# Kernel tuning notes

Hardware: AMD Instinct MI355X
Metric: run time of the kernel (lower is better)

Reference implementation:

```python
import jax, jax.numpy as jnp
import numpy as np

DIM = 64
NUM_USER = 100000
NUM_ITEM = 100000


def softmax_stable(x, mask=None, axis=-1):
    # exp(x - max) + 1e-10, optional multiplicative mask, normalize
    x = x - jax.lax.stop_gradient(jnp.max(x, axis=axis, keepdims=True))
    e = jnp.exp(x) + 1e-10
    if mask is not None:
        e = e * mask
    return e / jnp.sum(e, axis=axis, keepdims=True)


def setup_inputs() -> dict:
    key = jax.random.key(0)
    ks = jax.random.split(key, 16)
    B, S, L, N, dim = 32, 20, 50, 40000, DIM

    def emb_table(k, n):
        t = jax.random.normal(k, (n + 1, dim), jnp.float32) * 0.02
        return t.at[0].set(0.0)  # padding_idx=0

    def lin(k, fan_in, fan_out):
        s = 1.0 / np.sqrt(fan_in)
        kw, kb = jax.random.split(k)
        W = jax.random.uniform(kw, (fan_in, fan_out), jnp.float32, -s, s)
        b = jax.random.uniform(kb, (fan_out,), jnp.float32, -s, s)
        return W, b

    ue_w1, ue_b1 = lin(ks[7], 2 * dim, dim)      # attn_uencoder layer 1
    ue_w2, ue_b2 = lin(ks[8], dim, 1)            # attn_uencoder layer 2
    uenc_w, uenc_b = lin(ks[9], 2 * dim, dim)    # user_encoder_mlp
    pw, pb = lin(ks[10], 3 * dim, 1)             # predictor_mlp2

    return {
        "user_ids": jax.random.randint(ks[0], (B,), 1, NUM_USER + 1),
        "sess_item": jax.random.randint(ks[1], (B, S), 1, NUM_ITEM + 1),
        "rcnt_item": jax.random.randint(ks[2], (B, L), 1, NUM_ITEM + 1),
        "items_to_predict": jax.random.randint(ks[3], (B, N), 1, NUM_ITEM + 1),
        "item_emb": emb_table(ks[4], NUM_ITEM),
        "user_emb": emb_table(ks[5], NUM_USER),
        "user_emb2": emb_table(ks[6], NUM_USER),
        "ue_w1": ue_w1, "ue_b1": ue_b1,
        "ue_w2": ue_w2, "ue_b2": ue_b2,
        "uenc_w": uenc_w, "uenc_b": uenc_b,
        "pred_w": pw[:, 0], "pred_b": pb[0],
    }


def _forward(user_ids, sess_item, rcnt_item, items_to_predict,
             item_emb, user_emb, user_emb2,
             ue_w1, ue_b1, ue_w2, ue_b2, uenc_w, uenc_b, pred_w, pred_b):
    dim = item_emb.shape[-1]

    # ---- user_encoder7: attention over recent items, fused with user emb ----
    uemb = user_emb[user_ids]                      # [B, d]
    hs = item_emb[rcnt_item]                       # [B, L, d]
    rmask = (rcnt_item != 0)[..., None].astype(hs.dtype)
    cat = jnp.concatenate([jnp.broadcast_to(uemb[:, None, :], hs.shape), hs], axis=-1)
    w = jax.nn.relu(cat @ ue_w1 + ue_b1) @ ue_w2 + ue_b2   # [B, L, 1]
    w = softmax_stable(w, rmask, axis=1)
    hr = jnp.sum(w * hs, axis=1)                   # [B, d]
    hu = jnp.concatenate([user_emb2[user_ids], hr], axis=-1) @ uenc_w + uenc_b  # [B, d]

    # ---- session_encoder (attn_last): self-attention over session items ----
    e = item_emb[sess_item]                        # [B, S, d]
    smask = (sess_item != 0)
    attn_mask = (smask[:, :, None] & smask[:, None, :]).astype(e.dtype)
    logits = jnp.einsum('bsd,btd->bst', e, e) / jnp.sqrt(jnp.asarray(dim, e.dtype))
    a = softmax_stable(logits, attn_mask, axis=-1)
    hc = jnp.einsum('bst,btd->bsd', a, e)          # [B, S, d]

    # ---- predictor_attn, fused: Linear(3d,1) over the virtual [B,S,N,3d]
    # concat == three small projections + broadcast add (identical math) ----
    vemb = item_emb[items_to_predict]              # [B, N, d]
    wu, wc, wv = pred_w[:dim], pred_w[dim:2 * dim], pred_w[2 * dim:]
    g = (hu @ wu)[:, None, None] + (hc @ wc)[:, :, None] \
        + (vemb @ wv)[:, None, :] + pred_b          # [B, S, N]
    attn = jax.nn.sigmoid(g)

    # scores = ((attn*hu + (1-attn)*hc) * vemb).sum(-1), without building h
    hu_v = jnp.einsum('bd,bnd->bn', hu, vemb)       # [B, N]
    hc_v = jnp.einsum('bsd,bnd->bsn', hc, vemb)     # [B, S, N]
    scores = attn * hu_v[:, None, :] + (1.0 - attn) * hc_v
    return scores, hu, hc, attn[..., None]


def reference(user_ids, sess_item, rcnt_item, items_to_predict,
              item_emb, user_emb, user_emb2,
              ue_w1, ue_b1, ue_w2, ue_b2, uenc_w, uenc_b, pred_w, pred_b):
    return _forward(user_ids, sess_item, rcnt_item, items_to_predict,
                    item_emb, user_emb, user_emb2,
                    ue_w1, ue_b1, ue_w2, ue_b2, uenc_w, uenc_b, pred_w, pred_b)
```

## Files before the change

kernel.cpp:

```cpp
#include <hip/hip_runtime.h>
#include <hip/hip_bf16.h>
#include <math.h>

#define BB 32
#define SS 20
#define LL 50
#define NN 40000
#define DD 64
#define TBL_ROWS 100001

#define OFF_SCORES 0
#define OFF_HU     (BB * SS * NN)
#define OFF_HC     (OFF_HU + BB * DD)
#define OFF_ATTN   (OFF_HC + BB * SS * DD)

#define WS_COMB_OFF 4096
#define WS_TBL_OFF  (WS_COMB_OFF + BB * 32 * DD * 2)
#define WS_NEEDED   ((size_t)WS_TBL_OFF + (size_t)TBL_ROWS * DD * 2)
#define CONV_BLOCKS ((TBL_ROWS * 16 + 511) / 512)

typedef short  short8 __attribute__((ext_vector_type(8)));
typedef float  f32x16 __attribute__((ext_vector_type(16)));

__device__ __forceinline__ unsigned short f2bf(float x) {
    unsigned u = __float_as_uint(x);
    return (unsigned short)((u + 0x7fffu + ((u >> 16) & 1u)) >> 16);
}
__device__ __forceinline__ unsigned cvtpk(float lo, float hi) {
    unsigned r;
    asm("v_cvt_pk_bf16_f32 %0, %1, %2" : "=v"(r) : "v"(lo), "v"(hi));
    return r;
}
__device__ __forceinline__ short8 pack8_hw(float4 x, float4 y) {
    uint4 iv;
    iv.x = cvtpk(x.x, x.y); iv.y = cvtpk(x.z, x.w);
    iv.z = cvtpk(y.x, y.y); iv.w = cvtpk(y.z, y.w);
    return __builtin_bit_cast(short8, iv);
}

__global__ __launch_bounds__(512) void setup_kernel(
    const int* __restrict__ user_ids,
    const int* __restrict__ sess_item,
    const int* __restrict__ rcnt_item,
    const float* __restrict__ item_emb,
    const float* __restrict__ user_emb,
    const float* __restrict__ user_emb2,
    const float* __restrict__ ue_w1,
    const float* __restrict__ ue_b1,
    const float* __restrict__ ue_w2,
    const float* __restrict__ ue_b2,
    const float* __restrict__ uenc_w,
    const float* __restrict__ uenc_b,
    const float* __restrict__ pred_w,
    const float* __restrict__ pred_b,
    float* __restrict__ out,
    float* __restrict__ hcwc_ws,
    unsigned short* __restrict__ comb_bf,
    unsigned int* __restrict__ tbl_dst,
    int has_tbl)
{
    const int tid  = threadIdx.x;
    const int lane = tid & 63;
    const int wv   = tid >> 6;

    __shared__ float w1_s[2 * DD][DD];
    __shared__ float uemb_s[DD];
    __shared__ float u2_s[DD];
    __shared__ float hs_s[LL][DD];
    __shared__ float wraw_s[LL];
    __shared__ float wn_s[LL];
    __shared__ float part_s[8][DD];
    __shared__ float hr_s[DD];
    __shared__ float hu_s[DD];
    __shared__ float e_s[SS][DD + 1];
    __shared__ float a_tmp[8][SS];

    if (blockIdx.x >= 64u) {
        const int i = (blockIdx.x - 64) * 512 + tid;
        if (i < TBL_ROWS * 16) {
            float4 v = ((const float4*)item_emb)[i];
            ((uint2*)tbl_dst)[i] = make_uint2(cvtpk(v.x, v.y), cvtpk(v.z, v.w));
        }
        return;
    }

    if (blockIdx.x < 32u) {
        const int b = blockIdx.x;

        for (int t = tid; t < 2 * DD * DD / 4; t += 512)
            ((float4*)&w1_s[0][0])[t] = ((const float4*)ue_w1)[t];

        const int uid = user_ids[b];
        if (tid < DD) {
            uemb_s[tid] = user_emb[(size_t)uid * DD + tid];
            u2_s[tid]   = user_emb2[(size_t)uid * DD + tid];
        }
        for (int t = tid; t < LL * DD; t += 512) {
            int l = t >> 6, d = t & 63;
            int idx = rcnt_item[b * LL + l];
            hs_s[l][d] = item_emb[(size_t)idx * DD + d];
        }
        __syncthreads();

        float pu = 0.f;
        #pragma unroll 8
        for (int i = 0; i < DD; ++i) pu += uemb_s[i] * w1_s[i][lane];
        const float b1j = ue_b1[lane];
        const float w2j = ue_w2[lane];
        const float b2  = ue_b2[0];
        for (int l = wv; l < LL; l += 8) {
            float acc = pu + b1j;
            #pragma unroll 8
            for (int i = 0; i < DD; ++i) acc += hs_s[l][i] * w1_s[DD + i][lane];
            acc = fmaxf(acc, 0.f);
            float contrib = acc * w2j;
            #pragma unroll
            for (int off = 32; off; off >>= 1) contrib += __shfl_xor(contrib, off);
            if (lane == 0) wraw_s[l] = contrib + b2;
        }
        __syncthreads();

        if (wv == 0) {
            float x = (lane < LL) ? wraw_s[lane] : -INFINITY;
            float m = x;
            #pragma unroll
            for (int off = 32; off; off >>= 1) m = fmaxf(m, __shfl_xor(m, off));
            float maskl = (lane < LL && rcnt_item[b * LL + lane] != 0) ? 1.f : 0.f;
            float e = (lane < LL) ? (__expf(x - m) + 1e-10f) * maskl : 0.f;
            float sum = e;
            #pragma unroll
            for (int off = 32; off; off >>= 1) sum += __shfl_xor(sum, off);
            if (lane < LL) wn_s[lane] = e / sum;
        }
        __syncthreads();

        {
            float p = 0.f;
            for (int l = wv; l < LL; l += 8) p += wn_s[l] * hs_s[l][lane];
            part_s[wv][lane] = p;
        }
        __syncthreads();
        if (wv == 0) {
            float h = 0.f;
            #pragma unroll
            for (int w = 0; w < 8; ++w) h += part_s[w][lane];
            hr_s[lane] = h;
        }
        __syncthreads();

        {
            float p = 0.f;
            for (int i = wv * 16; i < wv * 16 + 16; ++i) {
                float c = (i < DD) ? u2_s[i] : hr_s[i - DD];
                p += c * uenc_w[i * DD + lane];
            }
            part_s[wv][lane] = p;
        }
        __syncthreads();
        if (wv == 0) {
            float hu = uenc_b[lane];
            #pragma unroll
            for (int w = 0; w < 8; ++w) hu += part_s[w][lane];
            hu_s[lane] = hu;
            out[OFF_HU + b * DD + lane] = hu;
        }
        __syncthreads();

        if (wv == 1) {
            float p = hu_s[lane] * pred_w[lane];
            #pragma unroll
            for (int off = 32; off; off >>= 1) p += __shfl_xor(p, off);
            if (lane == 0) hcwc_ws[b * 32 + 24] = p + pred_b[0];
        }
        if (tid < 11) {
            int sl = (tid < 4) ? (20 + tid) : (21 + tid);
            hcwc_ws[b * 32 + sl] = 0.f;
        }
        if (has_tbl) {
            for (int t = tid; t < 12 * DD; t += 512) {
                int row = 20 + (t >> 6), d = t & 63;
                float v = (row == 20) ? hu_s[d]
                        : (row == 21) ? pred_w[2 * DD + d] : 0.f;
                comb_bf[b * (32 * DD) + row * DD + d] = f2bf(v);
            }
        }
        return;
    }

    {
        const int b = blockIdx.x - 32;

        for (int t = tid; t < SS * DD; t += 512) {
            int s = t >> 6, d = t & 63;
            int idx = sess_item[b * SS + s];
            e_s[s][d] = item_emb[(size_t)idx * DD + d];
        }
        __syncthreads();

        const float wcj = pred_w[DD + lane];
        for (int s = wv; s < SS; s += 8) {
            const int t = lane;
            float lt = -INFINITY;
            float maskt = 0.f;
            if (t < SS) {
                float dot = 0.f;
                #pragma unroll 8
                for (int d = 0; d < DD; ++d) dot += e_s[s][d] * e_s[t][d];
                lt = dot * 0.125f;
                maskt = (sess_item[b * SS + t] != 0) ? 1.f : 0.f;
            }
            float srow = (sess_item[b * SS + s] != 0) ? 1.f : 0.f;
            float m = lt;
            #pragma unroll
            for (int off = 32; off; off >>= 1) m = fmaxf(m, __shfl_xor(m, off));
            float e = (t < SS) ? (__expf(lt - m) + 1e-10f) * (maskt * srow) : 0.f;
            float sum = e;
            #pragma unroll
            for (int off = 32; off; off >>= 1) sum += __shfl_xor(sum, off);
            if (t < SS) a_tmp[wv][t] = e / sum;
            float hc = 0.f;
            #pragma unroll
            for (int tt = 0; tt < SS; ++tt) hc += a_tmp[wv][tt] * e_s[tt][lane];

            out[OFF_HC + (size_t)(b * SS + s) * DD + lane] = hc;
            if (has_tbl) comb_bf[b * (32 * DD) + s * DD + lane] = f2bf(hc);
            float p = hc * wcj;
            #pragma unroll
            for (int off = 32; off; off >>= 1) p += __shfl_xor(p, off);
            if (lane == 0) hcwc_ws[b * 32 + s] = p;
        }
        return;
    }
}

#define LOADB_TBL(dst, idx)                                              \
    {                                                                    \
        const unsigned short* brow_ = tbl + (size_t)(idx) * DD + hi * 8; \
        dst[0] = *(const short8*)(brow_ +  0);                           \
        dst[1] = *(const short8*)(brow_ + 16);                           \
        dst[2] = *(const short8*)(brow_ + 32);                           \
        dst[3] = *(const short8*)(brow_ + 48);                           \
    }
#define LOADB_F32(dst, idx)                                              \
    {                                                                    \
        const float* brow_ = item_emb + (size_t)(idx) * DD + hi * 8;     \
        const float4* p0_ = (const float4*)(brow_ +  0);                 \
        const float4* p1_ = (const float4*)(brow_ + 16);                 \
        const float4* p2_ = (const float4*)(brow_ + 32);                 \
        const float4* p3_ = (const float4*)(brow_ + 48);                 \
        dst[0] = pack8_hw(p0_[0], p0_[1]);                               \
        dst[1] = pack8_hw(p1_[0], p1_[1]);                               \
        dst[2] = pack8_hw(p2_[0], p2_[1]);                               \
        dst[3] = pack8_hw(p3_[0], p3_[1]);                               \
    }

template<bool USE_TBL>
__global__ __launch_bounds__(256, 4) void score_kernel(
    const int* __restrict__ items,
    const float* __restrict__ item_emb,
    const unsigned short* __restrict__ tbl,
    const unsigned short* __restrict__ comb_bf,
    const float* __restrict__ pred_w,
    const float* __restrict__ hcwc_ws,
    float* __restrict__ out)
{
    const int tid   = threadIdx.x;
    const int lane  = tid & 63;
    const int wv    = tid >> 6;
    const int b     = blockIdx.y;
    const int strip = blockIdx.x * 4 + wv;
    const int n0    = strip * 128;
    if (n0 >= NN) return;
    const int c  = lane & 31;
    const int hi = lane >> 5;

    short8 aF[4];
    if (USE_TBL) {
        const unsigned short* arow = comb_bf + b * (32 * DD) + c * DD + hi * 8;
        #pragma unroll
        for (int t = 0; t < 4; ++t) aF[t] = *(const short8*)(arow + t * 16);
    } else {
        const float* rp = (c < SS) ? (out + OFF_HC + ((size_t)b * SS + c) * DD)
                        : (c == 20) ? (out + OFF_HU + (size_t)b * DD)
                        : (c == 21) ? (pred_w + 2 * DD) : nullptr;
        #pragma unroll
        for (int t = 0; t < 4; ++t) {
            if (rp) {
                const float4* p4 = (const float4*)(rp + t * 16 + hi * 8);
                aF[t] = pack8_hw(p4[0], p4[1]);
            } else {
                uint4 z = make_uint4(0, 0, 0, 0);
                aF[t] = __builtin_bit_cast(short8, z);
            }
        }
    }

    float hcr[12];
    #pragma unroll
    for (int r = 0; r < 12; ++r) {
        int row = (r & 3) + 8 * (r >> 2) + 4 * hi;
        hcr[r] = hcwc_ws[b * 32 + row];
    }
    const float c0v = hcwc_ws[b * 32 + 24];

    int idxT[4];
    #pragma unroll
    for (int T = 0; T < 4; ++T) {
        int nt = n0 + T * 32;
        idxT[T] = (nt < NN) ? items[b * NN + nt + c] : 0;
    }

    short8 bf0[4], bf1[4], bf2[4], bf3[4];
    if (USE_TBL) {
        LOADB_TBL(bf0, idxT[0]); LOADB_TBL(bf1, idxT[1]);
        LOADB_TBL(bf2, idxT[2]); LOADB_TBL(bf3, idxT[3]);
    } else {
        LOADB_F32(bf0, idxT[0]); LOADB_F32(bf1, idxT[1]);
        LOADB_F32(bf2, idxT[2]); LOADB_F32(bf3, idxT[3]);
    }

    #pragma unroll
    for (int T = 0; T < 4; ++T) {
        const int n0t = n0 + T * 32;
        if (n0t >= NN) continue;

        f32x16 acc = {0.f,0.f,0.f,0.f,0.f,0.f,0.f,0.f,0.f,0.f,0.f,0.f,0.f,0.f,0.f,0.f};
        #pragma unroll
        for (int t = 0; t < 4; ++t) {
            const short8 bfr = (T == 0) ? bf0[t] : (T == 1) ? bf1[t] : (T == 2) ? bf2[t] : bf3[t];
            acc = __builtin_amdgcn_mfma_f32_32x32x16_bf16(aF[t], bfr, acc, 0, 0, 0);
        }

        const float huv = __shfl(acc[8], 32 + c);
        const float vwv = __shfl(acc[9], 32 + c);
        const float gb  = c0v + vwv;

        float* sc = out + OFF_SCORES + (size_t)b * SS * NN + n0t + c;
        float* at = out + OFF_ATTN   + (size_t)b * SS * NN + n0t + c;

        #pragma unroll
        for (int r = 0; r < 12; ++r) {
            if (!(hi && r >= 8)) {
                int row = (r & 3) + 8 * (r >> 2) + 4 * hi;
                float hcv  = acc[r];
                float g    = gb + hcr[r];
                float attn = 1.f / (1.f + __expf(-g));
                float scv  = hcv + attn * (huv - hcv);
                sc[(size_t)row * NN] = scv;
                at[(size_t)row * NN] = attn;
            }
        }
    }
}

extern "C" void kernel_launch(void* const* d_in, const int* in_sizes, int n_in,
                              void* d_out, int out_size, void* d_ws, size_t ws_size,
                              hipStream_t stream) {
    const int*   user_ids  = (const int*)d_in[0];
    const int*   sess_item = (const int*)d_in[1];
    const int*   rcnt_item = (const int*)d_in[2];
    const int*   items     = (const int*)d_in[3];
    const float* item_emb  = (const float*)d_in[4];
    const float* user_emb  = (const float*)d_in[5];
    const float* user_emb2 = (const float*)d_in[6];
    const float* ue_w1     = (const float*)d_in[7];
    const float* ue_b1     = (const float*)d_in[8];
    const float* ue_w2     = (const float*)d_in[9];
    const float* ue_b2     = (const float*)d_in[10];
    const float* uenc_w    = (const float*)d_in[11];
    const float* uenc_b    = (const float*)d_in[12];
    const float* pred_w    = (const float*)d_in[13];
    const float* pred_b    = (const float*)d_in[14];
    float* out = (float*)d_out;

    float*          hcwc_ws = (float*)d_ws;
    unsigned short* comb_bf = (unsigned short*)((char*)d_ws + WS_COMB_OFF);
    unsigned short* tbl     = (unsigned short*)((char*)d_ws + WS_TBL_OFF);
    const bool use_tbl = (ws_size >= WS_NEEDED);
    const int  convB   = use_tbl ? CONV_BLOCKS : 0;

    hipLaunchKernelGGL(setup_kernel, dim3(64 + convB), dim3(512), 0, stream,
                       user_ids, sess_item, rcnt_item, item_emb, user_emb, user_emb2,
                       ue_w1, ue_b1, ue_w2, ue_b2, uenc_w, uenc_b, pred_w, pred_b,
                       out, hcwc_ws, comb_bf, (unsigned int*)tbl,
                       use_tbl ? 1 : 0);

    const int nstrips = (NN + 127) / 128;
    const dim3 grid((nstrips + 3) / 4, BB);
    if (use_tbl) {
        hipLaunchKernelGGL((score_kernel<true>), grid, dim3(256), 0, stream,
                           items, item_emb, tbl, comb_bf, pred_w, hcwc_ws, out);
    } else {
        hipLaunchKernelGGL((score_kernel<false>), grid, dim3(256), 0, stream,
                           items, item_emb, tbl, comb_bf, pred_w, hcwc_ws, out);
    }
}
```

Baseline: 82.21 us.

## Swap MFMA operands so each lane writes contiguous float4 rows of scores

Swaps the MFMA A/B operands so the accumulator holds items along rows and session slots along lanes. Each lane can then emit 16-byte vector stores of four consecutive items for scores and attn, instead of scalar stores strided by NN. hu·v and v·wv are now fetched with per-element shuffles from lanes 20/21, which adds 32 shuffles per tile. Lanes for unused slots (c>=20) do compute but skip their stores.

```diff
diff --git a/kernel.cpp b/kernel.cpp
--- a/kernel.cpp
+++ b/kernel.cpp
@@ -21,6 +21,7 @@
 
 typedef short  short8 __attribute__((ext_vector_type(8)));
 typedef float  f32x16 __attribute__((ext_vector_type(16)));
+typedef float  f32x4  __attribute__((ext_vector_type(4)));
 
 __device__ __forceinline__ unsigned short f2bf(float x) {
     unsigned u = __float_as_uint(x);
@@ -274,11 +275,11 @@
     const int c  = lane & 31;
     const int hi = lane >> 5;
 
-    short8 aF[4];
+    short8 combF[4];
     if (USE_TBL) {
         const unsigned short* arow = comb_bf + b * (32 * DD) + c * DD + hi * 8;
         #pragma unroll
-        for (int t = 0; t < 4; ++t) aF[t] = *(const short8*)(arow + t * 16);
+        for (int t = 0; t < 4; ++t) combF[t] = *(const short8*)(arow + t * 16);
     } else {
         const float* rp = (c < SS) ? (out + OFF_HC + ((size_t)b * SS + c) * DD)
                         : (c == 20) ? (out + OFF_HU + (size_t)b * DD)
@@ -287,21 +288,16 @@
         for (int t = 0; t < 4; ++t) {
             if (rp) {
                 const float4* p4 = (const float4*)(rp + t * 16 + hi * 8);
-                aF[t] = pack8_hw(p4[0], p4[1]);
+                combF[t] = pack8_hw(p4[0], p4[1]);
             } else {
                 uint4 z = make_uint4(0, 0, 0, 0);
-                aF[t] = __builtin_bit_cast(short8, z);
-            }
-        }
-    }
-
-    float hcr[12];
-    #pragma unroll
-    for (int r = 0; r < 12; ++r) {
-        int row = (r & 3) + 8 * (r >> 2) + 4 * hi;
-        hcr[r] = hcwc_ws[b * 32 + row];
-    }
-    const float c0v = hcwc_ws[b * 32 + 24];
+                combF[t] = __builtin_bit_cast(short8, z);
+            }
+        }
+    }
+
+    const float hcwcL = (c < SS) ? hcwc_ws[b * 32 + c] : 0.f;
+    const float c0v   = hcwc_ws[b * 32 + 24];
 
     int idxT[4];
     #pragma unroll
@@ -328,26 +324,30 @@
         #pragma unroll
         for (int t = 0; t < 4; ++t) {
             const short8 bfr = (T == 0) ? bf0[t] : (T == 1) ? bf1[t] : (T == 2) ? bf2[t] : bf3[t];
-            acc = __builtin_amdgcn_mfma_f32_32x32x16_bf16(aF[t], bfr, acc, 0, 0, 0);
-        }
-
-        const float huv = __shfl(acc[8], 32 + c);
-        const float vwv = __shfl(acc[9], 32 + c);
-        const float gb  = c0v + vwv;
-
-        float* sc = out + OFF_SCORES + (size_t)b * SS * NN + n0t + c;
-        float* at = out + OFF_ATTN   + (size_t)b * SS * NN + n0t + c;
+            acc = __builtin_amdgcn_mfma_f32_32x32x16_bf16(bfr, combF[t], acc, 0, 0, 0);
+        }
+
+        float* sc = out + OFF_SCORES + ((size_t)b * SS + c) * NN + n0t;
+        float* at = out + OFF_ATTN   + ((size_t)b * SS + c) * NN + n0t;
 
         #pragma unroll
-        for (int r = 0; r < 12; ++r) {
-            if (!(hi && r >= 8)) {
-                int row = (r & 3) + 8 * (r >> 2) + 4 * hi;
-                float hcv  = acc[r];
-                float g    = gb + hcr[r];
+        for (int q = 0; q < 4; ++q) {
+            f32x4 s4, a4;
+            #pragma unroll
+            for (int l = 0; l < 4; ++l) {
+                const int r = 4 * q + l;
+                float hcv = acc[r];
+                float huv = __shfl(acc[r], 20 + 32 * hi);
+                float vwv = __shfl(acc[r], 21 + 32 * hi);
+                float g    = c0v + vwv + hcwcL;
                 float attn = 1.f / (1.f + __expf(-g));
-                float scv  = hcv + attn * (huv - hcv);
-                sc[(size_t)row * NN] = scv;
-                at[(size_t)row * NN] = attn;
+                s4[l] = hcv + attn * (huv - hcv);
+                a4[l] = attn;
+            }
+            if (c < SS) {
+                const int nloc = 8 * q + 4 * hi;
+                *(f32x4*)(sc + nloc) = s4;
+                *(f32x4*)(at + nloc) = a4;
             }
         }
     }
```

New measurement: 94.25 us. 1.15x slower.
